# Kernel optimization log

Hardware: AMD Instinct MI355X
Metric: run time of the kernel (lower is better)

Reference implementation:

```python
import jax, jax.numpy as jnp
import numpy as np

B, N, D = 32768, 20, 13  # batch, n_humans, rotated-state dim (last input channel is mask)
LAYERS = {
    'm1': [(D, 150), (150, 100)],          # mlp1, last_relu=True
    'm2': [(100, 100), (100, 50)],          # mlp2
    'at': [(200, 100), (100, 100), (100, 1)],  # attention (global state concat -> 2*100 in)
    'hp': [(100, 100), (100, 100), (100, 7)],  # human_state_predictor (50*2 in)
}

def _mlp(x, params, last_relu=False):
    n = len(params)
    for i, (W, b) in enumerate(params):
        x = x @ W + b
        if i < n - 1 or last_relu:
            x = jax.nn.relu(x)
    return x

def setup_inputs() -> dict:
    key = jax.random.key(0)
    ks, kx, km = jax.random.split(key, 3)
    inp = {}
    for name, shapes in LAYERS.items():
        for i, (fi, fo) in enumerate(shapes):
            kw, kb, ks = jax.random.split(jax.random.fold_in(ks, i), 3)
            inp[f'{name}_w{i}'] = jax.random.normal(kw, (fi, fo), jnp.float32) / jnp.sqrt(float(fi))
            inp[f'{name}_b{i}'] = jnp.zeros((fo,), jnp.float32)
    x = jax.random.normal(kx, (B, N, D + 1), jnp.float32)
    mask = (jax.random.uniform(km, (B, N)) < 0.9).astype(jnp.float32)  # 0/1 visibility mask
    inp['state'] = x.at[..., -1].set(mask)
    return inp

def reference(state, m1_w0, m1_b0, m1_w1, m1_b1,
              m2_w0, m2_b0, m2_w1, m2_b1,
              at_w0, at_b0, at_w1, at_b1, at_w2, at_b2,
              hp_w0, hp_b0, hp_w1, hp_b1, hp_w2, hp_b2):
    x, mask = state[..., :-1], state[..., -1]        # (B,N,D), (B,N)
    h1 = _mlp(x, [(m1_w0, m1_b0), (m1_w1, m1_b1)], last_relu=True)   # (B,N,100)
    h2 = _mlp(h1, [(m2_w0, m2_b0), (m2_w1, m2_b1)])                   # (B,N,50)

    # masked mean-pool global state (NaN-on-empty zeroed, as in torch)
    msum = jnp.sum(mask, axis=1, keepdims=True)                       # (B,1)
    mw = jnp.where(msum > 0, mask / jnp.where(msum > 0, msum, 1.0), 0.0)
    global_state = jnp.sum(mw[..., None] * h1, axis=1, keepdims=True) # (B,1,100)
    att_in = jnp.concatenate([h1, jnp.broadcast_to(global_state, h1.shape)], axis=-1)

    scores = _mlp(att_in, [(at_w0, at_b0), (at_w1, at_b1), (at_w2, at_b2)])[..., 0]  # (B,N)
    scores = scores * mask
    se = jnp.exp(scores) * (scores != 0).astype(scores.dtype)
    ssum = jnp.sum(se, axis=1, keepdims=True)
    w = jnp.where(ssum > 0, se / jnp.where(ssum > 0, ssum, 1.0), 0.0)[..., None]  # (B,N,1)

    wsum = jnp.sum(w * h2, axis=1, keepdims=True)                     # (B,1,50)
    joint = jnp.concatenate([h2, jnp.broadcast_to(wsum, h2.shape)], axis=-1)  # (B,N,100)
    return _mlp(joint, [(hp_w0, hp_b0), (hp_w1, hp_b1), (hp_w2, hp_b2)])      # (B,N,7)
```

## Files before the change

kernel.cpp:

```cpp
#include <hip/hip_runtime.h>


typedef short sx8 __attribute__((ext_vector_type(8)));
typedef short sx4 __attribute__((ext_vector_type(4)));
typedef float fx4 __attribute__((ext_vector_type(4)));

#define TB   1024
#define NW   16
#define MTOK 160
#define CHH  1280

#define OFF_BUFT 0
#define OFF_BUFA 51200
#define OFF_BUFH 92160
#define OFF_BIAS 112640
#define OFF_GRC  116032
#define OFF_WRC  119232
#define OFF_SC   122432
#define OFF_MASK 123072
#define OFF_MSUM 123712
#define OFF_SSUM 123744
#define SMEM_BYTES 123776

#define B_M1B0 0
#define B_M1B1 152
#define B_M2B0 256
#define B_M2B1 360
#define B_ATB0 416
#define B_ATB1 520
#define B_HPB0 624
#define B_HPB1 728
#define B_HPB2 832

#define WS_M1W0 0
#define WS_M1W1 5120
#define WS_M2W0 23040
#define WS_M2W1 37376
#define WS_ATW0 45568
#define WS_ATW1 59904
#define WS_HPW0 74240
#define WS_HPW1 81408
#define WS_HPW2 95744

__device__ __forceinline__ short f2b(float f) {
    unsigned u = __builtin_bit_cast(unsigned, f);
    u += 0x7FFFu + ((u >> 16) & 1u);
    return (short)(u >> 16);
}
__device__ __forceinline__ float b2f(short h) {
    unsigned u = ((unsigned)(unsigned short)h) << 16;
    return __builtin_bit_cast(float, u);
}

__device__ __forceinline__ void stg(const float* __restrict__ W, int N,
                                    int KR, int KPAD, int NR, int Nsrc,
                                    short* dst, int gtid, int gsz) {
    int K8 = KPAD >> 3;
    for (int idx = gtid; idx < NR * K8; idx += gsz) {
        int k8 = idx / NR, nl = idx - k8 * NR;
        int k0 = k8 << 3;
        sx8 h;
        #pragma unroll
        for (int i = 0; i < 8; ++i) {
            int k = k0 + i;
            float v = (k < KR && nl < Nsrc) ? W[k * N + nl] : 0.f;
            h[i] = f2b(v);
        }
        *(sx8*)(dst + (k8 * NR + nl) * 8) = h;
    }
}

__global__ void stage_weights(
    const float* __restrict__ m1w0, const float* __restrict__ m1w1,
    const float* __restrict__ m2w0, const float* __restrict__ m2w1,
    const float* __restrict__ atw0, const float* __restrict__ atw1,
    const float* __restrict__ hpw0, const float* __restrict__ hpw1,
    const float* __restrict__ hpw2, short* __restrict__ ws)
{
    int gtid = blockIdx.x * blockDim.x + threadIdx.x;
    int gsz = gridDim.x * blockDim.x;
    stg(m1w0, 150, 13, 32, 160, 150, ws + WS_M1W0, gtid, gsz);
    stg(m1w1, 100, 150, 160, 112, 100, ws + WS_M1W1, gtid, gsz);
    stg(m2w0, 100, 100, 128, 112, 100, ws + WS_M2W0, gtid, gsz);
    stg(m2w1, 50, 100, 128, 64, 50, ws + WS_M2W1, gtid, gsz);
    stg(atw0, 100, 100, 128, 112, 100, ws + WS_ATW0, gtid, gsz);
    stg(atw1, 100, 100, 128, 112, 100, ws + WS_ATW1, gtid, gsz);
    stg(hpw0, 100, 50, 64, 112, 100, ws + WS_HPW0, gtid, gsz);
    stg(hpw1, 100, 100, 128, 112, 100, ws + WS_HPW1, gtid, gsz);
    stg(hpw2, 7, 100, 128, 16, 7, ws + WS_HPW2, gtid, gsz);
}

template <int KT, int NT, bool RELU, bool UINIT>
__device__ __forceinline__ void gemm(const short* __restrict__ wg, int NR,
                                     const short* bIn, short* bOut,
                                     const float* initp, int initBstride,
                                     int Nreal, int wave, int lm, int lq) {
    constexpr int NG = (NT + 1) / 2;
    for (int u = wave; u < NG * 5; u += NW) {
        int ng = u / 5, mg = u - ng * 5;
        int nt0 = ng * 2, nt1 = nt0 + 1;
        bool hasN1 = !((NT & 1) && (ng == NG - 1));
        sx8 a0[KT], a1[KT];
        #pragma unroll
        for (int kt = 0; kt < KT; ++kt)
            a0[kt] = *(const sx8*)(wg + ((kt * 4 + lq) * NR + nt0 * 16 + lm) * 8);
        if (hasN1) {
            #pragma unroll
            for (int kt = 0; kt < KT; ++kt)
                a1[kt] = *(const sx8*)(wg + ((kt * 4 + lq) * NR + nt1 * 16 + lm) * 8);
        }
        int n0l0 = nt0 * 16 + lq * 4;
        int n0l1 = nt1 * 16 + lq * 4;
        fx4 ib0, ib1;
        if (UINIT) {
            ib0 = *(const fx4*)(initp + n0l0);
            if (hasN1) ib1 = *(const fx4*)(initp + n0l1);
        }
        #pragma unroll
        for (int mi = 0; mi < 2; ++mi) {
            int mt = mg * 2 + mi;
            int tok = mt * 16 + lm;
            sx8 bfr[KT];
            #pragma unroll
            for (int kt = 0; kt < KT; ++kt)
                bfr[kt] = *(const sx8*)(bIn + (kt * 4 + lq) * CHH + tok * 8);
            fx4 acc0, acc1;
            if (UINIT) acc0 = ib0;
            else acc0 = *(const fx4*)(initp + (tok / 20) * initBstride + n0l0);
            if (hasN1) {
                if (UINIT) acc1 = ib1;
                else acc1 = *(const fx4*)(initp + (tok / 20) * initBstride + n0l1);
            }
            #pragma unroll
            for (int kt = 0; kt < KT; ++kt) {
                acc0 = __builtin_amdgcn_mfma_f32_16x16x32_bf16(a0[kt], bfr[kt], acc0, 0, 0, 0);
                if (hasN1)
                    acc1 = __builtin_amdgcn_mfma_f32_16x16x32_bf16(a1[kt], bfr[kt], acc1, 0, 0, 0);
            }
            sx4 hv;
            #pragma unroll
            for (int r = 0; r < 4; ++r) {
                float v = acc0[r];
                if (RELU) v = fmaxf(v, 0.f);
                if (n0l0 + r >= Nreal) v = 0.f;
                hv[r] = f2b(v);
            }
            *(sx4*)(bOut + (nt0 * 2 + (lq >> 1)) * CHH + tok * 8 + (lq & 1) * 4) = hv;
            if (hasN1) {
                #pragma unroll
                for (int r = 0; r < 4; ++r) {
                    float v = acc1[r];
                    if (RELU) v = fmaxf(v, 0.f);
                    if (n0l1 + r >= Nreal) v = 0.f;
                    hv[r] = f2b(v);
                }
                *(sx4*)(bOut + (nt1 * 2 + (lq >> 1)) * CHH + tok * 8 + (lq & 1) * 4) = hv;
            }
        }
    }
}

__device__ __forceinline__ void zpad(short* buf, int tid) {
    for (int i = tid; i < 320; i += TB) {
        sx8 z = {0, 0, 0, 0, 0, 0, 0, 0};
        *(sx8*)(buf + 14 * CHH + i * 8) = z;
    }
}

__global__ __launch_bounds__(TB, 4) void sp_mfma_bf16(
    const float* __restrict__ state,
    const float* __restrict__ m1b0, const float* __restrict__ m1b1,
    const float* __restrict__ m2b0, const float* __restrict__ m2b1,
    const float* __restrict__ atw0, const float* __restrict__ atb0,
    const float* __restrict__ atb1,
    const float* __restrict__ atw2, const float* __restrict__ atb2,
    const float* __restrict__ hpw0, const float* __restrict__ hpb0,
    const float* __restrict__ hpb1, const float* __restrict__ hpb2,
    const short* __restrict__ ws,
    float* __restrict__ out)
{
    __shared__ __align__(16) unsigned char smem[SMEM_BYTES];
    short* bufT  = (short*)(smem + OFF_BUFT);
    short* bufA  = (short*)(smem + OFF_BUFA);
    short* bufH2 = (short*)(smem + OFF_BUFH);
    float* biasv = (float*)(smem + OFF_BIAS);
    float* grc   = (float*)(smem + OFF_GRC);
    float* wrc   = (float*)(smem + OFF_WRC);
    float* scv   = (float*)(smem + OFF_SC);
    float* maskv = (float*)(smem + OFF_MASK);
    float* msum  = (float*)(smem + OFF_MSUM);
    float* ssum  = (float*)(smem + OFF_SSUM);

    const int tid  = threadIdx.x;
    const int lane = tid & 63;
    const int wave = tid >> 6;
    const int lm   = lane & 15;
    const int lq   = lane >> 4;
    const long gt0 = (long)blockIdx.x * MTOK;

    {
        const float* bs[9] = {m1b0, m1b1, m2b0, m2b1, atb0, atb1, hpb0, hpb1, hpb2};
        const int off[9] = {B_M1B0, B_M1B1, B_M2B0, B_M2B1, B_ATB0, B_ATB1, B_HPB0, B_HPB1, B_HPB2};
        const int sz[9]  = {150, 100, 100, 50, 100, 100, 100, 100, 7};
        const int pd[9]  = {152, 104, 104, 56, 104, 104, 104, 104, 16};
        #pragma unroll
        for (int r = 0; r < 9; ++r)
            for (int i = tid; i < pd[r]; i += TB)
                biasv[off[r] + i] = (i < sz[r]) ? bs[r][i] : 0.f;
        if (tid < MTOK) maskv[tid] = state[(gt0 + tid) * 14 + 13];
        for (int idx = tid; idx < MTOK * 4; idx += TB) {
            int row = idx >> 2, seg = idx & 3;
            const float* xp = state + (gt0 + row) * 14;
            sx8 h;
            #pragma unroll
            for (int i = 0; i < 8; ++i) {
                int k = seg * 8 + i;
                float v = (k < 13) ? xp[k] : 0.f;
                h[i] = f2b(v);
            }
            *(sx8*)(bufA + seg * CHH + row * 8) = h;
        }
    }
    __syncthreads();

    if (tid < 8) {
        float s = 0.f;
        #pragma unroll
        for (int n = 0; n < 20; ++n) s += maskv[tid * 20 + n];
        msum[tid] = s;
    }
    gemm<1, 10, true, true>(ws + WS_M1W0, 160, bufA, bufT, biasv + B_M1B0, 0,
                            150, wave, lm, lq);
    __syncthreads();

    gemm<5, 7, true, true>(ws + WS_M1W1, 112, bufT, bufA, biasv + B_M1B1, 0,
                           100, wave, lm, lq);
    zpad(bufA, tid);
    __syncthreads();

    for (int task = tid; task < 800; task += TB) {
        int b = task / 100, j = task - b * 100;
        float ms = msum[b];
        float inv = (ms > 0.f) ? 1.f / ms : 0.f;
        float a = 0.f;
        #pragma unroll
        for (int n = 0; n < 20; ++n)
            a = fmaf(maskv[b * 20 + n], b2f(bufA[(j >> 3) * CHH + (b * 20 + n) * 8 + (j & 7)]), a);
        grc[task] = a * inv;
    }
    __syncthreads();

    {
        float g0 = 0.f;
        if (tid < 800) {
            int b = tid / 100, j = tid - b * 100;
            float a = biasv[B_ATB0 + j];
            #pragma unroll 10
            for (int k = 0; k < 100; ++k)
                a = fmaf(grc[b * 100 + k], atw0[(100 + k) * 100 + j], a);
            g0 = a;
        }
        __syncthreads();
        if (tid < 800) grc[tid] = g0;
    }
    __syncthreads();

    gemm<4, 7, true, true>(ws + WS_M2W0, 112, bufA, bufT, biasv + B_M2B0, 0,
                           100, wave, lm, lq);
    zpad(bufT, tid);
    __syncthreads();

    gemm<4, 4, false, true>(ws + WS_M2W1, 64, bufT, bufH2, biasv + B_M2B1, 0,
                            50, wave, lm, lq);
    __syncthreads();

    gemm<4, 7, true, false>(ws + WS_ATW0, 112, bufA, bufT, grc, 100,
                            100, wave, lm, lq);
    __syncthreads();

    gemm<4, 7, true, true>(ws + WS_ATW1, 112, bufT, bufA, biasv + B_ATB1, 0,
                           100, wave, lm, lq);
    __syncthreads();

    if (tid < MTOK) {
        float s = atb2[0];
        #pragma unroll
        for (int k8 = 0; k8 < 13; ++k8) {
            sx8 v = *(const sx8*)(bufA + k8 * CHH + tid * 8);
            #pragma unroll
            for (int i = 0; i < 8; ++i) {
                int k = k8 * 8 + i;
                if (k < 100) s = fmaf(b2f(v[i]), atw2[k], s);
            }
        }
        s *= maskv[tid];
        scv[tid] = (s != 0.f) ? __expf(s) : 0.f;
    }
    __syncthreads();
    if (tid < 8) {
        float s = 0.f;
        #pragma unroll
        for (int n = 0; n < 20; ++n) s += scv[tid * 20 + n];
        ssum[tid] = s;
    }
    __syncthreads();

    if (tid < 400) {
        int b = tid / 50, j = tid - b * 50;
        float ss = ssum[b];
        float inv = (ss > 0.f) ? 1.f / ss : 0.f;
        float a = 0.f;
        #pragma unroll
        for (int n = 0; n < 20; ++n)
            a = fmaf(scv[b * 20 + n], b2f(bufH2[(j >> 3) * CHH + (b * 20 + n) * 8 + (j & 7)]), a);
        wrc[b * 50 + j] = a * inv;
    }
    __syncthreads();

    {
        float g0 = 0.f;
        if (tid < 800) {
            int b = tid / 100, j = tid - b * 100;
            float a = biasv[B_HPB0 + j];
            #pragma unroll 10
            for (int k = 0; k < 50; ++k)
                a = fmaf(wrc[b * 50 + k], hpw0[(50 + k) * 100 + j], a);
            g0 = a;
        }
        __syncthreads();
        if (tid < 800) wrc[tid] = g0;
    }
    __syncthreads();

    gemm<2, 7, true, false>(ws + WS_HPW0, 112, bufH2, bufT, wrc, 100,
                            100, wave, lm, lq);
    __syncthreads();

    gemm<4, 7, true, true>(ws + WS_HPW1, 112, bufT, bufA, biasv + B_HPB1, 0,
                           100, wave, lm, lq);
    __syncthreads();

    {
        sx8 afr[4];
        #pragma unroll
        for (int kt = 0; kt < 4; ++kt)
            afr[kt] = *(const sx8*)(ws + WS_HPW2 + ((kt * 4 + lq) * 16 + lm) * 8);
        fx4 ib = *(const fx4*)(biasv + B_HPB2 + lq * 4);
        for (int mt = wave; mt < 10; mt += NW) {
            int tok = mt * 16 + lm;
            fx4 acc = ib;
            const short* bp = bufA + tok * 8;
            #pragma unroll
            for (int kt = 0; kt < 4; ++kt) {
                sx8 b = *(const sx8*)(bp + (kt * 4 + lq) * CHH);
                acc = __builtin_amdgcn_mfma_f32_16x16x32_bf16(afr[kt], b, acc, 0, 0, 0);
            }
            #pragma unroll
            for (int r = 0; r < 4; ++r) {
                int n = lq * 4 + r;
                if (n < 7) out[(gt0 + tok) * 7 + n] = acc[r];
            }
        }
    }
}

extern "C" void kernel_launch(void* const* d_in, const int* in_sizes, int n_in,
                              void* d_out, int out_size, void* d_ws, size_t ws_size,
                              hipStream_t stream) {
    int si = 20, wb = 0;
    if (in_sizes[0] > 1000000) { si = 0; wb = 1; }
    const float* state = (const float*)d_in[si];
    const float* W[20];
    for (int i = 0; i < 20; ++i) W[i] = (const float*)d_in[wb + i];
    float* out = (float*)d_out;
    short* ws = (short*)d_ws;
    int Btot = in_sizes[si] / (20 * 14);
    int nblocks = Btot / 8;

    hipLaunchKernelGGL(stage_weights, dim3(128), dim3(256), 0, stream,
        W[0], W[2], W[4], W[6], W[8], W[10], W[14], W[16], W[18], ws);

    hipLaunchKernelGGL(sp_mfma_bf16, dim3(nblocks), dim3(TB), 0, stream,
        state,
        W[1], W[3],
        W[5], W[7],
        W[8], W[9],
        W[11],
        W[12], W[13],
        W[14], W[15],
        W[17], W[19],
        ws, out);
}
```

Measured before the change: 514.0 us.

## Halve block tile to 4 batches and move global-state projections onto MFMA

Each block now handles 4 batch items (80 tokens) with 512 threads instead of 8 items with 1024 threads, which roughly halves LDS use per block and doubles the block count. The per-batch global-state projections through the second halves of at_w0 and hp_w0 used scalar FMA loops over fp32 weights read from global memory. They now run as bf16 MFMA GEMMs (gemmR) on staged weight halves. The pooled vectors are rounded to bf16 first, which adds some error. The gemm tiling is adjusted for 5 M-tiles per block, with an odd last tile.

```diff
diff --git a/kernel.cpp b/kernel.cpp
--- a/kernel.cpp
+++ b/kernel.cpp
@@ -5,22 +5,26 @@
 typedef short sx4 __attribute__((ext_vector_type(4)));
 typedef float fx4 __attribute__((ext_vector_type(4)));
 
-#define TB   1024
-#define NW   16
-#define MTOK 160
-#define CHH  1280
+#define TB   512
+#define NW   8
+#define NB   4
+#define MTOK 80
+#define MT   5
+#define CHH  640
+#define CHG  128
 
 #define OFF_BUFT 0
-#define OFF_BUFA 51200
-#define OFF_BUFH 92160
-#define OFF_BIAS 112640
-#define OFF_GRC  116032
-#define OFF_WRC  119232
-#define OFF_SC   122432
-#define OFF_MASK 123072
-#define OFF_MSUM 123712
-#define OFF_SSUM 123744
-#define SMEM_BYTES 123776
+#define OFF_BUFA 25600
+#define OFF_BUFH 46080
+#define OFF_BUFG 56320
+#define OFF_BIAS 60416
+#define OFF_GRC  63808
+#define OFF_WRC  65408
+#define OFF_SC   67008
+#define OFF_MASK 67328
+#define OFF_MSUM 67648
+#define OFF_SSUM 67664
+#define SMEM_BYTES 67680
 
 #define B_M1B0 0
 #define B_M1B1 152
@@ -32,15 +36,17 @@
 #define B_HPB1 728
 #define B_HPB2 832
 
-#define WS_M1W0 0
-#define WS_M1W1 5120
-#define WS_M2W0 23040
-#define WS_M2W1 37376
-#define WS_ATW0 45568
-#define WS_ATW1 59904
-#define WS_HPW0 74240
-#define WS_HPW1 81408
-#define WS_HPW2 95744
+#define WS_M1W0  0
+#define WS_M1W1  5120
+#define WS_M2W0  23040
+#define WS_M2W1  37376
+#define WS_ATW0  45568
+#define WS_ATW1  59904
+#define WS_HPW0  74240
+#define WS_HPW1  81408
+#define WS_HPW2  95744
+#define WS_ATW0H 97792
+#define WS_HPW0H 112128
 
 __device__ __forceinline__ short f2b(float f) {
     unsigned u = __builtin_bit_cast(unsigned, f);
@@ -88,6 +94,8 @@
     stg(hpw0, 100, 50, 64, 112, 100, ws + WS_HPW0, gtid, gsz);
     stg(hpw1, 100, 100, 128, 112, 100, ws + WS_HPW1, gtid, gsz);
     stg(hpw2, 7, 100, 128, 16, 7, ws + WS_HPW2, gtid, gsz);
+    stg(atw0 + 100 * 100, 100, 100, 128, 112, 100, ws + WS_ATW0H, gtid, gsz);
+    stg(hpw0 + 50 * 100, 100, 50, 64, 112, 100, ws + WS_HPW0H, gtid, gsz);
 }
 
 template <int KT, int NT, bool RELU, bool UINIT>
@@ -96,8 +104,8 @@
                                      const float* initp, int initBstride,
                                      int Nreal, int wave, int lm, int lq) {
     constexpr int NG = (NT + 1) / 2;
-    for (int u = wave; u < NG * 5; u += NW) {
-        int ng = u / 5, mg = u - ng * 5;
+    for (int u = wave; u < NG * 3; u += NW) {
+        int ng = u / 3, mg = u - ng * 3;
         int nt0 = ng * 2, nt1 = nt0 + 1;
         bool hasN1 = !((NT & 1) && (ng == NG - 1));
         sx8 a0[KT], a1[KT];
@@ -116,8 +124,9 @@
             ib0 = *(const fx4*)(initp + n0l0);
             if (hasN1) ib1 = *(const fx4*)(initp + n0l1);
         }
-        #pragma unroll
-        for (int mi = 0; mi < 2; ++mi) {
+        int mcount = (mg == 2) ? 1 : 2;
+        #pragma unroll 2
+        for (int mi = 0; mi < mcount; ++mi) {
             int mt = mg * 2 + mi;
             int tok = mt * 16 + lm;
             sx8 bfr[KT];
@@ -160,8 +169,56 @@
     }
 }
 
+template <int KT, int NT>
+__device__ __forceinline__ void gemmR(const short* __restrict__ wg, int NR,
+                                      const short* bG, float* outF,
+                                      const float* biasp,
+                                      int wave, int lm, int lq) {
+    constexpr int NG = (NT + 1) / 2;
+    for (int u = wave; u < NG; u += NW) {
+        int nt0 = u * 2, nt1 = nt0 + 1;
+        bool hasN1 = !((NT & 1) && (u == NG - 1));
+        sx8 a0[KT], a1[KT], bfr[KT];
+        #pragma unroll
+        for (int kt = 0; kt < KT; ++kt) {
+            a0[kt] = *(const sx8*)(wg + ((kt * 4 + lq) * NR + nt0 * 16 + lm) * 8);
+            bfr[kt] = *(const sx8*)(bG + (kt * 4 + lq) * CHG + lm * 8);
+        }
+        if (hasN1) {
+            #pragma unroll
+            for (int kt = 0; kt < KT; ++kt)
+                a1[kt] = *(const sx8*)(wg + ((kt * 4 + lq) * NR + nt1 * 16 + lm) * 8);
+        }
+        int n0l0 = nt0 * 16 + lq * 4;
+        int n0l1 = nt1 * 16 + lq * 4;
+        fx4 acc0 = *(const fx4*)(biasp + n0l0);
+        fx4 acc1;
+        if (hasN1) acc1 = *(const fx4*)(biasp + n0l1);
+        #pragma unroll
+        for (int kt = 0; kt < KT; ++kt) {
+            acc0 = __builtin_amdgcn_mfma_f32_16x16x32_bf16(a0[kt], bfr[kt], acc0, 0, 0, 0);
+            if (hasN1)
+                acc1 = __builtin_amdgcn_mfma_f32_16x16x32_bf16(a1[kt], bfr[kt], acc1, 0, 0, 0);
+        }
+        if (lm < NB) {
+            #pragma unroll
+            for (int r = 0; r < 4; ++r) {
+                int n = n0l0 + r;
+                if (n < 100) outF[lm * 100 + n] = acc0[r];
+            }
+            if (hasN1) {
+                #pragma unroll
+                for (int r = 0; r < 4; ++r) {
+                    int n = n0l1 + r;
+                    if (n < 100) outF[lm * 100 + n] = acc1[r];
+                }
+            }
+        }
+    }
+}
+
 __device__ __forceinline__ void zpad(short* buf, int tid) {
-    for (int i = tid; i < 320; i += TB) {
+    for (int i = tid; i < 160; i += TB) {
         sx8 z = {0, 0, 0, 0, 0, 0, 0, 0};
         *(sx8*)(buf + 14 * CHH + i * 8) = z;
     }
@@ -171,11 +228,10 @@
     const float* __restrict__ state,
     const float* __restrict__ m1b0, const float* __restrict__ m1b1,
     const float* __restrict__ m2b0, const float* __restrict__ m2b1,
-    const float* __restrict__ atw0, const float* __restrict__ atb0,
-    const float* __restrict__ atb1,
+    const float* __restrict__ atb0, const float* __restrict__ atb1,
     const float* __restrict__ atw2, const float* __restrict__ atb2,
-    const float* __restrict__ hpw0, const float* __restrict__ hpb0,
-    const float* __restrict__ hpb1, const float* __restrict__ hpb2,
+    const float* __restrict__ hpb0, const float* __restrict__ hpb1,
+    const float* __restrict__ hpb2,
     const short* __restrict__ ws,
     float* __restrict__ out)
 {
@@ -183,6 +239,7 @@
     short* bufT  = (short*)(smem + OFF_BUFT);
     short* bufA  = (short*)(smem + OFF_BUFA);
     short* bufH2 = (short*)(smem + OFF_BUFH);
+    short* bufG  = (short*)(smem + OFF_BUFG);
     float* biasv = (float*)(smem + OFF_BIAS);
     float* grc   = (float*)(smem + OFF_GRC);
     float* wrc   = (float*)(smem + OFF_WRC);
@@ -223,7 +280,7 @@
     }
     __syncthreads();
 
-    if (tid < 8) {
+    if (tid < NB) {
         float s = 0.f;
         #pragma unroll
         for (int n = 0; n < 20; ++n) s += maskv[tid * 20 + n];
@@ -238,33 +295,26 @@
     zpad(bufA, tid);
     __syncthreads();
 
-    for (int task = tid; task < 800; task += TB) {
-        int b = task / 100, j = task - b * 100;
-        float ms = msum[b];
-        float inv = (ms > 0.f) ? 1.f / ms : 0.f;
-        float a = 0.f;
-        #pragma unroll
-        for (int n = 0; n < 20; ++n)
-            a = fmaf(maskv[b * 20 + n], b2f(bufA[(j >> 3) * CHH + (b * 20 + n) * 8 + (j & 7)]), a);
-        grc[task] = a * inv;
-    }
-    __syncthreads();
-
-    {
-        float g0 = 0.f;
-        if (tid < 800) {
-            int b = tid / 100, j = tid - b * 100;
-            float a = biasv[B_ATB0 + j];
-            #pragma unroll 10
-            for (int k = 0; k < 100; ++k)
-                a = fmaf(grc[b * 100 + k], atw0[(100 + k) * 100 + j], a);
-            g0 = a;
-        }
-        __syncthreads();
-        if (tid < 800) grc[tid] = g0;
-    }
-    __syncthreads();
-
+    for (int t = tid; t < 2048; t += TB) {
+        int c = t >> 7, rem = t & 127;
+        int tg = rem >> 3, h = rem & 7;
+        int j = c * 8 + h;
+        float v = 0.f;
+        if (tg < NB && j < 100) {
+            float ms = msum[tg];
+            float inv = (ms > 0.f) ? 1.f / ms : 0.f;
+            float a = 0.f;
+            #pragma unroll
+            for (int n = 0; n < 20; ++n)
+                a = fmaf(maskv[tg * 20 + n],
+                         b2f(bufA[(j >> 3) * CHH + (tg * 20 + n) * 8 + (j & 7)]), a);
+            v = a * inv;
+        }
+        bufG[t] = f2b(v);
+    }
+    __syncthreads();
+
+    gemmR<4, 7>(ws + WS_ATW0H, 112, bufG, grc, biasv + B_ATB0, wave, lm, lq);
     gemm<4, 7, true, true>(ws + WS_M2W0, 112, bufA, bufT, biasv + B_M2B0, 0,
                            100, wave, lm, lq);
     zpad(bufT, tid);
@@ -297,7 +347,7 @@
         scv[tid] = (s != 0.f) ? __expf(s) : 0.f;
     }
     __syncthreads();
-    if (tid < 8) {
+    if (tid < NB) {
         float s = 0.f;
         #pragma unroll
         for (int n = 0; n < 20; ++n) s += scv[tid * 20 + n];
@@ -305,31 +355,26 @@
     }
     __syncthreads();
 
-    if (tid < 400) {
-        int b = tid / 50, j = tid - b * 50;
-        float ss = ssum[b];
-        float inv = (ss > 0.f) ? 1.f / ss : 0.f;
-        float a = 0.f;
-        #pragma unroll
-        for (int n = 0; n < 20; ++n)
-            a = fmaf(scv[b * 20 + n], b2f(bufH2[(j >> 3) * CHH + (b * 20 + n) * 8 + (j & 7)]), a);
-        wrc[b * 50 + j] = a * inv;
-    }
-    __syncthreads();
-
-    {
-        float g0 = 0.f;
-        if (tid < 800) {
-            int b = tid / 100, j = tid - b * 100;
-            float a = biasv[B_HPB0 + j];
-            #pragma unroll 10
-            for (int k = 0; k < 50; ++k)
-                a = fmaf(wrc[b * 50 + k], hpw0[(50 + k) * 100 + j], a);
-            g0 = a;
-        }
-        __syncthreads();
-        if (tid < 800) wrc[tid] = g0;
-    }
+    for (int t = tid; t < 1024; t += TB) {
+        int c = t >> 7, rem = t & 127;
+        int tg = rem >> 3, h = rem & 7;
+        int j = c * 8 + h;
+        float v = 0.f;
+        if (tg < NB && j < 50) {
+            float ss = ssum[tg];
+            float inv = (ss > 0.f) ? 1.f / ss : 0.f;
+            float a = 0.f;
+            #pragma unroll
+            for (int n = 0; n < 20; ++n)
+                a = fmaf(scv[tg * 20 + n],
+                         b2f(bufH2[(j >> 3) * CHH + (tg * 20 + n) * 8 + (j & 7)]), a);
+            v = a * inv;
+        }
+        bufG[t] = f2b(v);
+    }
+    __syncthreads();
+
+    gemmR<2, 7>(ws + WS_HPW0H, 112, bufG, wrc, biasv + B_HPB0, wave, lm, lq);
     __syncthreads();
 
     gemm<2, 7, true, false>(ws + WS_HPW0, 112, bufH2, bufT, wrc, 100,
@@ -346,7 +391,7 @@
         for (int kt = 0; kt < 4; ++kt)
             afr[kt] = *(const sx8*)(ws + WS_HPW2 + ((kt * 4 + lq) * 16 + lm) * 8);
         fx4 ib = *(const fx4*)(biasv + B_HPB2 + lq * 4);
-        for (int mt = wave; mt < 10; mt += NW) {
+        for (int mt = wave; mt < MT; mt += NW) {
             int tok = mt * 16 + lm;
             fx4 acc = ib;
             const short* bp = bufA + tok * 8;
@@ -375,7 +420,7 @@
     float* out = (float*)d_out;
     short* ws = (short*)d_ws;
     int Btot = in_sizes[si] / (20 * 14);
-    int nblocks = Btot / 8;
+    int nblocks = Btot / NB;
 
     hipLaunchKernelGGL(stage_weights, dim3(128), dim3(256), 0, stream,
         W[0], W[2], W[4], W[6], W[8], W[10], W[14], W[16], W[18], ws);
@@ -384,10 +429,8 @@
         state,
         W[1], W[3],
         W[5], W[7],
-        W[8], W[9],
-        W[11],
+        W[9], W[11],
         W[12], W[13],
-        W[14], W[15],
-        W[17], W[19],
+        W[15], W[17], W[19],
         ws, out);
 }
```

Result: faster. 453.3 us (-11.8%).
